# Kernel optimization log

Hardware: AMD Instinct MI355X
Metric: run time of the kernel (lower is better)

The kernel has to match this reference:

```python
import jax, jax.numpy as jnp
import numpy as np

N = 50000
E = 800000
D = 64


def _gcn_layer(x, row, col, norm, W, b, n_nodes):
    # h = X W  (PyG GCNConv applies linear before propagation, bias after)
    h = x @ W                                   # [N, D]
    msg = norm[:, None] * h[row]                # gather source feats, [E+N, D]
    out = jax.ops.segment_sum(msg, col, num_segments=n_nodes)  # scatter to targets
    return out + b


def _gcn_norm(edge_index, n_nodes, dtype):
    # add self loops with weight 1, symmetric normalization D^-1/2 (A+I) D^-1/2
    sl = jnp.arange(n_nodes, dtype=edge_index.dtype)
    row = jnp.concatenate([edge_index[0], sl])  # source
    col = jnp.concatenate([edge_index[1], sl])  # target
    w = jnp.ones(row.shape[0], dtype=dtype)
    deg = jax.ops.segment_sum(w, col, num_segments=n_nodes)
    dinv = jnp.where(deg > 0, jax.lax.rsqrt(deg), 0.0)
    norm = dinv[row] * dinv[col]                # [E+N]
    return row, col, norm


def setup_inputs() -> dict:
    key = jax.random.key(0)
    k1, k2, k3, k4 = jax.random.split(key, 4)
    x = jax.random.normal(k1, (N, D), dtype=jnp.float32)
    edge_index = jax.random.randint(k2, (2, E), 0, N, dtype=jnp.int64)
    # Glorot-style init like PyG GCNConv lin weights; bias zeros
    s = 1.0 / np.sqrt(D)
    W1 = jax.random.uniform(k3, (D, D), jnp.float32, -s, s)
    W2 = jax.random.uniform(k4, (D, D), jnp.float32, -s, s)
    b1 = jnp.zeros((D,), jnp.float32)
    b2 = jnp.zeros((D,), jnp.float32)
    return {"x": x, "W1": W1, "b1": b1, "W2": W2, "b2": b2, "edge_index": edge_index}


def reference(x, W1, b1, W2, b2, edge_index):
    n_nodes = x.shape[0]
    row, col, norm = _gcn_norm(edge_index, n_nodes, x.dtype)
    z = _gcn_layer(x, row, col, norm, W1, b1, n_nodes)
    z = jax.nn.relu(z)
    z = _gcn_layer(z, row, col, norm, W2, b2, n_nodes)
    z = jax.nn.relu(z)
    return z
```

## Files before the change

### kernel.cpp

```cpp
#include <hip/hip_runtime.h>


#define DF 64
#define XS_LD 68
#define ECHUNK 4096
#define BCAP 5120

__device__ __forceinline__ unsigned short f2bf(float f) {
  union { float f; unsigned int u; } c; c.f = f;
  unsigned int r = c.u + 0x7FFFu + ((c.u >> 16) & 1u);
  return (unsigned short)(r >> 16);
}
__device__ __forceinline__ float bflo(unsigned int u) {
  union { unsigned int u; float f; } c; c.u = u << 16; return c.f;
}
__device__ __forceinline__ float bfhi(unsigned int u) {
  union { unsigned int u; float f; } c; c.u = u & 0xFFFF0000u; return c.f;
}

__global__ void init_cur_k(int* __restrict__ gcursor) {
  gcursor[threadIdx.x] = threadIdx.x * BCAP;
}

__global__ __launch_bounds__(256) void part_k(
    const int* __restrict__ rows, const int* __restrict__ cols,
    int* __restrict__ gcursor, unsigned int* __restrict__ bfile, int e_cnt)
{
  __shared__ int h[256];
  __shared__ int p[256];
  __shared__ int lb[256];
  __shared__ int cur[256];
  __shared__ int gb[256];
  __shared__ unsigned int buf[ECHUNK];
  const int tid = threadIdx.x;
  h[tid] = 0; __syncthreads();

  const int e0 = blockIdx.x * ECHUNK;
  const int m  = min(ECHUNK, e_cnt - e0);
  unsigned int pk[ECHUNK / 256];
  int bk[ECHUNK / 256];
#pragma unroll
  for (int j = 0; j < ECHUNK / 256; ++j) {
    int idx = j * 256 + tid;
    if (idx < m) {
      int c = cols[e0 + idx];
      int r = rows[e0 + idx];
      bk[j] = c >> 8;
      pk[j] = ((unsigned int)(c & 255) << 16) | (unsigned int)r;
      atomicAdd(&h[bk[j]], 1);
    } else bk[j] = -1;
  }
  __syncthreads();

  const int myc = h[tid];
  p[tid] = myc; __syncthreads();
  for (int off = 1; off < 256; off <<= 1) {
    int t = (tid >= off) ? p[tid - off] : 0;
    __syncthreads();
    p[tid] += t;
    __syncthreads();
  }
  const int ex = p[tid] - myc;
  lb[tid] = ex; cur[tid] = ex;
  if (myc > 0) gb[tid] = atomicAdd(&gcursor[tid], myc);
  __syncthreads();

#pragma unroll
  for (int j = 0; j < ECHUNK / 256; ++j)
    if (bk[j] >= 0) { int pos = atomicAdd(&cur[bk[j]], 1); buf[pos] = pk[j]; }
  __syncthreads();

  for (int i = tid; i < m; i += 256) {
    int lo = 0, hi = 255;
    while (lo < hi) { int mid = (lo + hi + 1) >> 1; if (lb[mid] <= i) lo = mid; else hi = mid - 1; }
    bfile[gb[lo] + (i - lb[lo])] = buf[i];
  }
}

__global__ __launch_bounds__(256) void bucket_k(
    const unsigned int* __restrict__ bfile, const int* __restrict__ gcursor,
    int* __restrict__ csr_src, int* __restrict__ basep, int* __restrict__ cntp,
    float* __restrict__ dinv, int n)
{
  __shared__ unsigned int ein[BCAP];
  __shared__ unsigned short eout[BCAP];
  __shared__ int h[256];
  __shared__ int p[256];
  __shared__ int cur[256];
  const int tid = threadIdx.x;
  const int b   = blockIdx.x;
  const int s   = b * BCAP;
  int L = gcursor[b] - s;
  if (L > BCAP) L = BCAP;

  for (int i = tid; i < L; i += 256) ein[i] = bfile[s + i];
  h[tid] = 0; __syncthreads();
  for (int i = tid; i < L; i += 256) atomicAdd(&h[(ein[i] >> 16) & 255], 1);
  __syncthreads();

  const int myc = h[tid];
  p[tid] = myc; __syncthreads();
  for (int off = 1; off < 256; off <<= 1) {
    int t = (tid >= off) ? p[tid - off] : 0;
    __syncthreads();
    p[tid] += t;
    __syncthreads();
  }
  const int ex = p[tid] - myc;
  cur[tid] = ex;
  __syncthreads();

  for (int i = tid; i < L; i += 256) {
    unsigned int pk = ein[i];
    int pos = atomicAdd(&cur[(pk >> 16) & 255], 1);
    eout[pos] = (unsigned short)(pk & 0xffffu);
  }
  __syncthreads();

  for (int i = tid; i < L; i += 256) csr_src[s + i] = (int)eout[i];

  const int node = b * 256 + tid;
  if (node < n) {
    basep[node] = s + ex;
    cntp[node]  = myc;
    dinv[node]  = rsqrtf(1.0f + (float)myc);
  }
}

__global__ __launch_bounds__(256) void conv_k(
    const float* __restrict__ x, const float* __restrict__ dinv,
    uint4* __restrict__ xh, int n)
{
  int t = blockIdx.x * blockDim.x + threadIdx.x;
  if (t >= n * 8) return;
  const float dv = dinv[t >> 3];
  float4 v0 = ((const float4*)x)[(size_t)t * 2 + 0];
  float4 v1 = ((const float4*)x)[(size_t)t * 2 + 1];
  uint4 o;
  o.x = (unsigned int)f2bf(dv * v0.x) | ((unsigned int)f2bf(dv * v0.y) << 16);
  o.y = (unsigned int)f2bf(dv * v0.z) | ((unsigned int)f2bf(dv * v0.w) << 16);
  o.z = (unsigned int)f2bf(dv * v1.x) | ((unsigned int)f2bf(dv * v1.y) << 16);
  o.w = (unsigned int)f2bf(dv * v1.z) | ((unsigned int)f2bf(dv * v1.w) << 16);
  xh[t] = o;
}

template<int OUTBF>
__global__ __launch_bounds__(256) void fused_layer_k(
    const uint4* __restrict__ inh, const float* __restrict__ W,
    const float* __restrict__ bias, const int* __restrict__ csr_src,
    const int* __restrict__ basep, const int* __restrict__ cntp,
    const float* __restrict__ dinv, void* __restrict__ outp, int n)
{
  __shared__ float Ws[DF * XS_LD];
  __shared__ float Ss[32 * XS_LD];
  const int tid = threadIdx.x;

#pragma unroll
  for (int i = 0; i < 4; ++i) {
    const int f4 = tid + 256 * i;
    const int k  = f4 >> 4;
    const int c0 = (f4 & 15) * 4;
    *(float4*)(Ws + k * XS_LD + c0) = *(const float4*)(W + (size_t)f4 * 4);
  }

  const int nl   = tid >> 3;
  const int q    = tid & 7;
  const int node = blockIdx.x * 32 + nl;
  const bool valid = (node < n);
  float dv = 0.f;

  if (valid) {
    float a[8] = {0,0,0,0,0,0,0,0};
    float b2[8] = {0,0,0,0,0,0,0,0};
    dv = dinv[node];
    {
      uint4 v = inh[(size_t)node * 8 + q];
      a[0] += bflo(v.x); a[1] += bfhi(v.x); a[2] += bflo(v.y); a[3] += bfhi(v.y);
      a[4] += bflo(v.z); a[5] += bfhi(v.z); a[6] += bflo(v.w); a[7] += bfhi(v.w);
    }
    const int s = basep[node], c = cntp[node];
    int k = 0;
    for (; k + 4 <= c; k += 4) {
      int r0 = csr_src[s + k + 0], r1 = csr_src[s + k + 1];
      int r2 = csr_src[s + k + 2], r3 = csr_src[s + k + 3];
      uint4 v0 = inh[(size_t)r0 * 8 + q];
      uint4 v1 = inh[(size_t)r1 * 8 + q];
      uint4 v2 = inh[(size_t)r2 * 8 + q];
      uint4 v3 = inh[(size_t)r3 * 8 + q];
      a[0]  += bflo(v0.x) + bflo(v1.x); a[1]  += bfhi(v0.x) + bfhi(v1.x);
      a[2]  += bflo(v0.y) + bflo(v1.y); a[3]  += bfhi(v0.y) + bfhi(v1.y);
      a[4]  += bflo(v0.z) + bflo(v1.z); a[5]  += bfhi(v0.z) + bfhi(v1.z);
      a[6]  += bflo(v0.w) + bflo(v1.w); a[7]  += bfhi(v0.w) + bfhi(v1.w);
      b2[0] += bflo(v2.x) + bflo(v3.x); b2[1] += bfhi(v2.x) + bfhi(v3.x);
      b2[2] += bflo(v2.y) + bflo(v3.y); b2[3] += bfhi(v2.y) + bfhi(v3.y);
      b2[4] += bflo(v2.z) + bflo(v3.z); b2[5] += bfhi(v2.z) + bfhi(v3.z);
      b2[6] += bflo(v2.w) + bflo(v3.w); b2[7] += bfhi(v2.w) + bfhi(v3.w);
    }
    for (; k < c; ++k) {
      int r = csr_src[s + k];
      uint4 v = inh[(size_t)r * 8 + q];
      a[0] += bflo(v.x); a[1] += bfhi(v.x); a[2] += bflo(v.y); a[3] += bfhi(v.y);
      a[4] += bflo(v.z); a[5] += bfhi(v.z); a[6] += bflo(v.w); a[7] += bfhi(v.w);
    }
    float4 s0 = make_float4(dv * (a[0] + b2[0]), dv * (a[1] + b2[1]),
                            dv * (a[2] + b2[2]), dv * (a[3] + b2[3]));
    float4 s1 = make_float4(dv * (a[4] + b2[4]), dv * (a[5] + b2[5]),
                            dv * (a[6] + b2[6]), dv * (a[7] + b2[7]));
    *(float4*)(Ss + nl * XS_LD + q * 8 + 0) = s0;
    *(float4*)(Ss + nl * XS_LD + q * 8 + 4) = s1;
  }
  __syncthreads();

  float4 o0 = ((const float4*)bias)[q * 2 + 0];
  float4 o1 = ((const float4*)bias)[q * 2 + 1];
#pragma unroll 16
  for (int k = 0; k < DF; ++k) {
    const float sk = Ss[nl * XS_LD + k];
    const float4 w0 = *(const float4*)(Ws + k * XS_LD + q * 8 + 0);
    const float4 w1 = *(const float4*)(Ws + k * XS_LD + q * 8 + 4);
    o0.x += sk * w0.x; o0.y += sk * w0.y; o0.z += sk * w0.z; o0.w += sk * w0.w;
    o1.x += sk * w1.x; o1.y += sk * w1.y; o1.z += sk * w1.z; o1.w += sk * w1.w;
  }
  if (valid) {
    o0.x = fmaxf(o0.x, 0.f); o0.y = fmaxf(o0.y, 0.f);
    o0.z = fmaxf(o0.z, 0.f); o0.w = fmaxf(o0.w, 0.f);
    o1.x = fmaxf(o1.x, 0.f); o1.y = fmaxf(o1.y, 0.f);
    o1.z = fmaxf(o1.z, 0.f); o1.w = fmaxf(o1.w, 0.f);
    if (OUTBF) {
      uint4 u;
      u.x = (unsigned int)f2bf(dv * o0.x) | ((unsigned int)f2bf(dv * o0.y) << 16);
      u.y = (unsigned int)f2bf(dv * o0.z) | ((unsigned int)f2bf(dv * o0.w) << 16);
      u.z = (unsigned int)f2bf(dv * o1.x) | ((unsigned int)f2bf(dv * o1.y) << 16);
      u.w = (unsigned int)f2bf(dv * o1.z) | ((unsigned int)f2bf(dv * o1.w) << 16);
      ((uint4*)outp)[(size_t)node * 8 + q] = u;
    } else {
      ((float4*)outp)[(size_t)node * 16 + q * 2 + 0] = o0;
      ((float4*)outp)[(size_t)node * 16 + q * 2 + 1] = o1;
    }
  }
}

extern "C" void kernel_launch(void* const* d_in, const int* in_sizes, int n_in,
                              void* d_out, int out_size, void* d_ws, size_t ws_size,
                              hipStream_t stream) {
  const float* x  = (const float*)d_in[0];
  const float* W1 = (const float*)d_in[1];
  const float* b1 = (const float*)d_in[2];
  const float* W2 = (const float*)d_in[3];
  const float* b2 = (const float*)d_in[4];
  const int*   ei = (const int*)d_in[5];

  const int n = in_sizes[0] / DF;
  const int E = in_sizes[5] / 2;
  const int* rows = ei;
  const int* cols = ei + E;
  const int nb = (n + 255) >> 8;
  const int eblocks = (E + ECHUNK - 1) / ECHUNK;

  char* w = (char*)d_ws;
  size_t off = 0;
  auto alloc = [&](size_t bytes) { char* p = w + off; off = (off + bytes + 255) & ~(size_t)255; return p; };
  float* dinv    = (float*)alloc((size_t)n * 4);
  int*   cntp    = (int*)  alloc((size_t)n * 4);
  int*   basep   = (int*)  alloc((size_t)n * 4);
  int*   gcursor = (int*)  alloc(256 * 4);
  unsigned int* bfile = (unsigned int*)alloc((size_t)nb * BCAP * 4);
  int*   csr_src = (int*)  alloc((size_t)nb * BCAP * 4);
  uint4* xh      = (uint4*)alloc((size_t)n * DF * 2);
  uint4* zh      = (uint4*)alloc((size_t)n * DF * 2);

  const int b256 = 256;

  init_cur_k<<<1, 256, 0, stream>>>(gcursor);
  part_k<<<eblocks, b256, 0, stream>>>(rows, cols, gcursor, bfile, E);
  bucket_k<<<nb, b256, 0, stream>>>(bfile, gcursor, csr_src, basep, cntp, dinv, n);

  conv_k<<<(n * 8 + 255) / 256, b256, 0, stream>>>(x, dinv, xh, n);

  const int lay_blocks = (n + 31) / 32;

  fused_layer_k<1><<<lay_blocks, b256, 0, stream>>>(xh, W1, b1, csr_src, basep, cntp, dinv, zh, n);
  fused_layer_k<0><<<lay_blocks, b256, 0, stream>>>(zh, W2, b2, csr_src, basep, cntp, dinv, d_out, n);
}
```

Baseline: 93.53 us.

## Split bf16 features into column halves and gather each half in separate passes

```diff
diff --git a/kernel.cpp b/kernel.cpp
--- a/kernel.cpp
+++ b/kernel.cpp
@@ -5,6 +5,8 @@
 #define XS_LD 68
 #define ECHUNK 4096
 #define BCAP 5120
+
+typedef float vf4 __attribute__((ext_vector_type(4)));
 
 __device__ __forceinline__ unsigned short f2bf(float f) {
   union { float f; unsigned int u; } c; c.f = f;
@@ -46,7 +48,7 @@
       int c = cols[e0 + idx];
       int r = rows[e0 + idx];
       bk[j] = c >> 8;
-      pk[j] = ((unsigned int)(c & 255) << 16) | (unsigned int)r;
+      pk[j] = ((unsigned int)bk[j] << 24) | ((unsigned int)(c & 255) << 16) | (unsigned int)r;
       atomicAdd(&h[bk[j]], 1);
     } else bk[j] = -1;
   }
@@ -71,9 +73,9 @@
   __syncthreads();
 
   for (int i = tid; i < m; i += 256) {
-    int lo = 0, hi = 255;
-    while (lo < hi) { int mid = (lo + hi + 1) >> 1; if (lb[mid] <= i) lo = mid; else hi = mid - 1; }
-    bfile[gb[lo] + (i - lb[lo])] = buf[i];
+    unsigned int v = buf[i];
+    int b = (int)(v >> 24);
+    bfile[gb[b] + (i - lb[b])] = v;
   }
 }
 
@@ -129,11 +131,12 @@
 
 __global__ __launch_bounds__(256) void conv_k(
     const float* __restrict__ x, const float* __restrict__ dinv,
-    uint4* __restrict__ xh, int n)
+    uint4* __restrict__ xlo, uint4* __restrict__ xhi, int n)
 {
   int t = blockIdx.x * blockDim.x + threadIdx.x;
   if (t >= n * 8) return;
-  const float dv = dinv[t >> 3];
+  const int node = t >> 3, q = t & 7;
+  const float dv = dinv[node];
   float4 v0 = ((const float4*)x)[(size_t)t * 2 + 0];
   float4 v1 = ((const float4*)x)[(size_t)t * 2 + 1];
   uint4 o;
@@ -141,101 +144,165 @@
   o.y = (unsigned int)f2bf(dv * v0.z) | ((unsigned int)f2bf(dv * v0.w) << 16);
   o.z = (unsigned int)f2bf(dv * v1.x) | ((unsigned int)f2bf(dv * v1.y) << 16);
   o.w = (unsigned int)f2bf(dv * v1.z) | ((unsigned int)f2bf(dv * v1.w) << 16);
-  xh[t] = o;
+  if (q < 4) xlo[(size_t)node * 4 + q] = o;
+  else       xhi[(size_t)node * 4 + (q - 4)] = o;
+}
+
+__global__ __launch_bounds__(256) void gatherA_k(
+    const uint4* __restrict__ inlo, const int* __restrict__ csr_src,
+    const int* __restrict__ basep, const int* __restrict__ cntp,
+    const float* __restrict__ dinv, float* __restrict__ Slo, int n)
+{
+  const int nl = threadIdx.x >> 2;
+  const int q  = threadIdx.x & 3;
+  const int node = blockIdx.x * 64 + nl;
+  if (node >= n) return;
+
+  float a[8], b[8];
+  {
+    uint4 v = inlo[(size_t)node * 4 + q];
+    a[0] = bflo(v.x); a[1] = bfhi(v.x); a[2] = bflo(v.y); a[3] = bfhi(v.y);
+    a[4] = bflo(v.z); a[5] = bfhi(v.z); a[6] = bflo(v.w); a[7] = bfhi(v.w);
+#pragma unroll
+    for (int j = 0; j < 8; ++j) b[j] = 0.f;
+  }
+  const int s = basep[node], c = cntp[node];
+  int k = 0;
+  for (; k + 4 <= c; k += 4) {
+    int r0 = __builtin_nontemporal_load(csr_src + s + k + 0);
+    int r1 = __builtin_nontemporal_load(csr_src + s + k + 1);
+    int r2 = __builtin_nontemporal_load(csr_src + s + k + 2);
+    int r3 = __builtin_nontemporal_load(csr_src + s + k + 3);
+    uint4 v0 = inlo[(size_t)r0 * 4 + q];
+    uint4 v1 = inlo[(size_t)r1 * 4 + q];
+    uint4 v2 = inlo[(size_t)r2 * 4 + q];
+    uint4 v3 = inlo[(size_t)r3 * 4 + q];
+    a[0] += bflo(v0.x) + bflo(v1.x); a[1] += bfhi(v0.x) + bfhi(v1.x);
+    a[2] += bflo(v0.y) + bflo(v1.y); a[3] += bfhi(v0.y) + bfhi(v1.y);
+    a[4] += bflo(v0.z) + bflo(v1.z); a[5] += bfhi(v0.z) + bfhi(v1.z);
+    a[6] += bflo(v0.w) + bflo(v1.w); a[7] += bfhi(v0.w) + bfhi(v1.w);
+    b[0] += bflo(v2.x) + bflo(v3.x); b[1] += bfhi(v2.x) + bfhi(v3.x);
+    b[2] += bflo(v2.y) + bflo(v3.y); b[3] += bfhi(v2.y) + bfhi(v3.y);
+    b[4] += bflo(v2.z) + bflo(v3.z); b[5] += bfhi(v2.z) + bfhi(v3.z);
+    b[6] += bflo(v2.w) + bflo(v3.w); b[7] += bfhi(v2.w) + bfhi(v3.w);
+  }
+  for (; k < c; ++k) {
+    int r = __builtin_nontemporal_load(csr_src + s + k);
+    uint4 v = inlo[(size_t)r * 4 + q];
+    a[0] += bflo(v.x); a[1] += bfhi(v.x); a[2] += bflo(v.y); a[3] += bfhi(v.y);
+    a[4] += bflo(v.z); a[5] += bfhi(v.z); a[6] += bflo(v.w); a[7] += bfhi(v.w);
+  }
+  const float dv = dinv[node];
+  vf4 o0 = {dv*(a[0]+b[0]), dv*(a[1]+b[1]), dv*(a[2]+b[2]), dv*(a[3]+b[3])};
+  vf4 o1 = {dv*(a[4]+b[4]), dv*(a[5]+b[5]), dv*(a[6]+b[6]), dv*(a[7]+b[7])};
+  __builtin_nontemporal_store(o0, (vf4*)(Slo + (size_t)node * 32 + q * 8 + 0));
+  __builtin_nontemporal_store(o1, (vf4*)(Slo + (size_t)node * 32 + q * 8 + 4));
 }
 
 template<int OUTBF>
-__global__ __launch_bounds__(256) void fused_layer_k(
-    const uint4* __restrict__ inh, const float* __restrict__ W,
-    const float* __restrict__ bias, const int* __restrict__ csr_src,
-    const int* __restrict__ basep, const int* __restrict__ cntp,
-    const float* __restrict__ dinv, void* __restrict__ outp, int n)
+__global__ __launch_bounds__(256) void gatherB_gemm_k(
+    const uint4* __restrict__ inhi, const float* __restrict__ Slo,
+    const float* __restrict__ W, const float* __restrict__ bias,
+    const int* __restrict__ csr_src, const int* __restrict__ basep,
+    const int* __restrict__ cntp, const float* __restrict__ dinv,
+    void* __restrict__ out0, void* __restrict__ out1, int n)
 {
   __shared__ float Ws[DF * XS_LD];
-  __shared__ float Ss[32 * XS_LD];
+  __shared__ float Ss[64 * XS_LD];
   const int tid = threadIdx.x;
 
 #pragma unroll
   for (int i = 0; i < 4; ++i) {
     const int f4 = tid + 256 * i;
-    const int k  = f4 >> 4;
+    const int kk = f4 >> 4;
     const int c0 = (f4 & 15) * 4;
-    *(float4*)(Ws + k * XS_LD + c0) = *(const float4*)(W + (size_t)f4 * 4);
-  }
-
-  const int nl   = tid >> 3;
-  const int q    = tid & 7;
-  const int node = blockIdx.x * 32 + nl;
-  const bool valid = (node < n);
-  float dv = 0.f;
-
-  if (valid) {
-    float a[8] = {0,0,0,0,0,0,0,0};
-    float b2[8] = {0,0,0,0,0,0,0,0};
-    dv = dinv[node];
+    *(float4*)(Ws + kk * XS_LD + c0) = *(const float4*)(W + (size_t)f4 * 4);
+  }
+
+  const int nl = tid >> 2;
+  const int q  = tid & 3;
+  const int node = blockIdx.x * 64 + nl;
+
+  if (node < n) {
+    float a[8], b[8];
     {
-      uint4 v = inh[(size_t)node * 8 + q];
-      a[0] += bflo(v.x); a[1] += bfhi(v.x); a[2] += bflo(v.y); a[3] += bfhi(v.y);
-      a[4] += bflo(v.z); a[5] += bfhi(v.z); a[6] += bflo(v.w); a[7] += bfhi(v.w);
+      uint4 v = inhi[(size_t)node * 4 + q];
+      a[0] = bflo(v.x); a[1] = bfhi(v.x); a[2] = bflo(v.y); a[3] = bfhi(v.y);
+      a[4] = bflo(v.z); a[5] = bfhi(v.z); a[6] = bflo(v.w); a[7] = bfhi(v.w);
+#pragma unroll
+      for (int j = 0; j < 8; ++j) b[j] = 0.f;
     }
     const int s = basep[node], c = cntp[node];
     int k = 0;
     for (; k + 4 <= c; k += 4) {
-      int r0 = csr_src[s + k + 0], r1 = csr_src[s + k + 1];
-      int r2 = csr_src[s + k + 2], r3 = csr_src[s + k + 3];
-      uint4 v0 = inh[(size_t)r0 * 8 + q];
-      uint4 v1 = inh[(size_t)r1 * 8 + q];
-      uint4 v2 = inh[(size_t)r2 * 8 + q];
-      uint4 v3 = inh[(size_t)r3 * 8 + q];
-      a[0]  += bflo(v0.x) + bflo(v1.x); a[1]  += bfhi(v0.x) + bfhi(v1.x);
-      a[2]  += bflo(v0.y) + bflo(v1.y); a[3]  += bfhi(v0.y) + bfhi(v1.y);
-      a[4]  += bflo(v0.z) + bflo(v1.z); a[5]  += bfhi(v0.z) + bfhi(v1.z);
-      a[6]  += bflo(v0.w) + bflo(v1.w); a[7]  += bfhi(v0.w) + bfhi(v1.w);
-      b2[0] += bflo(v2.x) + bflo(v3.x); b2[1] += bfhi(v2.x) + bfhi(v3.x);
-      b2[2] += bflo(v2.y) + bflo(v3.y); b2[3] += bfhi(v2.y) + bfhi(v3.y);
-      b2[4] += bflo(v2.z) + bflo(v3.z); b2[5] += bfhi(v2.z) + bfhi(v3.z);
-      b2[6] += bflo(v2.w) + bflo(v3.w); b2[7] += bfhi(v2.w) + bfhi(v3.w);
+      int r0 = __builtin_nontemporal_load(csr_src + s + k + 0);
+      int r1 = __builtin_nontemporal_load(csr_src + s + k + 1);
+      int r2 = __builtin_nontemporal_load(csr_src + s + k + 2);
+      int r3 = __builtin_nontemporal_load(csr_src + s + k + 3);
+      uint4 v0 = inhi[(size_t)r0 * 4 + q];
+      uint4 v1 = inhi[(size_t)r1 * 4 + q];
+      uint4 v2 = inhi[(size_t)r2 * 4 + q];
+      uint4 v3 = inhi[(size_t)r3 * 4 + q];
+      a[0] += bflo(v0.x) + bflo(v1.x); a[1] += bfhi(v0.x) + bfhi(v1.x);
+      a[2] += bflo(v0.y) + bflo(v1.y); a[3] += bfhi(v0.y) + bfhi(v1.y);
+      a[4] += bflo(v0.z) + bflo(v1.z); a[5] += bfhi(v0.z) + bfhi(v1.z);
+      a[6] += bflo(v0.w) + bflo(v1.w); a[7] += bfhi(v0.w) + bfhi(v1.w);
+      b[0] += bflo(v2.x) + bflo(v3.x); b[1] += bfhi(v2.x) + bfhi(v3.x);
+      b[2] += bflo(v2.y) + bflo(v3.y); b[3] += bfhi(v2.y) + bfhi(v3.y);
+      b[4] += bflo(v2.z) + bflo(v3.z); b[5] += bfhi(v2.z) + bfhi(v3.z);
+      b[6] += bflo(v2.w) + bflo(v3.w); b[7] += bfhi(v2.w) + bfhi(v3.w);
     }
     for (; k < c; ++k) {
-      int r = csr_src[s + k];
-      uint4 v = inh[(size_t)r * 8 + q];
+      int r = __builtin_nontemporal_load(csr_src + s + k);
+      uint4 v = inhi[(size_t)r * 4 + q];
       a[0] += bflo(v.x); a[1] += bfhi(v.x); a[2] += bflo(v.y); a[3] += bfhi(v.y);
       a[4] += bflo(v.z); a[5] += bfhi(v.z); a[6] += bflo(v.w); a[7] += bfhi(v.w);
     }
-    float4 s0 = make_float4(dv * (a[0] + b2[0]), dv * (a[1] + b2[1]),
-                            dv * (a[2] + b2[2]), dv * (a[3] + b2[3]));
-    float4 s1 = make_float4(dv * (a[4] + b2[4]), dv * (a[5] + b2[5]),
-                            dv * (a[6] + b2[6]), dv * (a[7] + b2[7]));
-    *(float4*)(Ss + nl * XS_LD + q * 8 + 0) = s0;
-    *(float4*)(Ss + nl * XS_LD + q * 8 + 4) = s1;
-  }
-  __syncthreads();
-
-  float4 o0 = ((const float4*)bias)[q * 2 + 0];
-  float4 o1 = ((const float4*)bias)[q * 2 + 1];
+    const float dv = dinv[node];
+    float4 h0 = make_float4(dv*(a[0]+b[0]), dv*(a[1]+b[1]), dv*(a[2]+b[2]), dv*(a[3]+b[3]));
+    float4 h1 = make_float4(dv*(a[4]+b[4]), dv*(a[5]+b[5]), dv*(a[6]+b[6]), dv*(a[7]+b[7]));
+    *(float4*)(Ss + nl * XS_LD + 32 + q * 8 + 0) = h0;
+    *(float4*)(Ss + nl * XS_LD + 32 + q * 8 + 4) = h1;
+    vf4 l0 = __builtin_nontemporal_load((const vf4*)(Slo + (size_t)node * 32 + q * 8 + 0));
+    vf4 l1 = __builtin_nontemporal_load((const vf4*)(Slo + (size_t)node * 32 + q * 8 + 4));
+    *(vf4*)(Ss + nl * XS_LD + q * 8 + 0) = l0;
+    *(vf4*)(Ss + nl * XS_LD + q * 8 + 4) = l1;
+  }
+  __syncthreads();
+
+  const int q2 = tid & 7;
+#pragma unroll
+  for (int sub = 0; sub < 2; ++sub) {
+    const int nl2 = (tid >> 3) + 32 * sub;
+    const int node2 = blockIdx.x * 64 + nl2;
+    float4 o0 = ((const float4*)bias)[q2 * 2 + 0];
+    float4 o1 = ((const float4*)bias)[q2 * 2 + 1];
 #pragma unroll 16
-  for (int k = 0; k < DF; ++k) {
-    const float sk = Ss[nl * XS_LD + k];
-    const float4 w0 = *(const float4*)(Ws + k * XS_LD + q * 8 + 0);
-    const float4 w1 = *(const float4*)(Ws + k * XS_LD + q * 8 + 4);
-    o0.x += sk * w0.x; o0.y += sk * w0.y; o0.z += sk * w0.z; o0.w += sk * w0.w;
-    o1.x += sk * w1.x; o1.y += sk * w1.y; o1.z += sk * w1.z; o1.w += sk * w1.w;
-  }
-  if (valid) {
-    o0.x = fmaxf(o0.x, 0.f); o0.y = fmaxf(o0.y, 0.f);
-    o0.z = fmaxf(o0.z, 0.f); o0.w = fmaxf(o0.w, 0.f);
-    o1.x = fmaxf(o1.x, 0.f); o1.y = fmaxf(o1.y, 0.f);
-    o1.z = fmaxf(o1.z, 0.f); o1.w = fmaxf(o1.w, 0.f);
-    if (OUTBF) {
-      uint4 u;
-      u.x = (unsigned int)f2bf(dv * o0.x) | ((unsigned int)f2bf(dv * o0.y) << 16);
-      u.y = (unsigned int)f2bf(dv * o0.z) | ((unsigned int)f2bf(dv * o0.w) << 16);
-      u.z = (unsigned int)f2bf(dv * o1.x) | ((unsigned int)f2bf(dv * o1.y) << 16);
-      u.w = (unsigned int)f2bf(dv * o1.z) | ((unsigned int)f2bf(dv * o1.w) << 16);
-      ((uint4*)outp)[(size_t)node * 8 + q] = u;
-    } else {
-      ((float4*)outp)[(size_t)node * 16 + q * 2 + 0] = o0;
-      ((float4*)outp)[(size_t)node * 16 + q * 2 + 1] = o1;
+    for (int k = 0; k < DF; ++k) {
+      const float sk = Ss[nl2 * XS_LD + k];
+      const float4 w0 = *(const float4*)(Ws + k * XS_LD + q2 * 8 + 0);
+      const float4 w1 = *(const float4*)(Ws + k * XS_LD + q2 * 8 + 4);
+      o0.x += sk * w0.x; o0.y += sk * w0.y; o0.z += sk * w0.z; o0.w += sk * w0.w;
+      o1.x += sk * w1.x; o1.y += sk * w1.y; o1.z += sk * w1.z; o1.w += sk * w1.w;
+    }
+    if (node2 < n) {
+      o0.x = fmaxf(o0.x, 0.f); o0.y = fmaxf(o0.y, 0.f);
+      o0.z = fmaxf(o0.z, 0.f); o0.w = fmaxf(o0.w, 0.f);
+      o1.x = fmaxf(o1.x, 0.f); o1.y = fmaxf(o1.y, 0.f);
+      o1.z = fmaxf(o1.z, 0.f); o1.w = fmaxf(o1.w, 0.f);
+      if (OUTBF) {
+        const float dv2 = dinv[node2];
+        uint4 u;
+        u.x = (unsigned int)f2bf(dv2 * o0.x) | ((unsigned int)f2bf(dv2 * o0.y) << 16);
+        u.y = (unsigned int)f2bf(dv2 * o0.z) | ((unsigned int)f2bf(dv2 * o0.w) << 16);
+        u.z = (unsigned int)f2bf(dv2 * o1.x) | ((unsigned int)f2bf(dv2 * o1.y) << 16);
+        u.w = (unsigned int)f2bf(dv2 * o1.z) | ((unsigned int)f2bf(dv2 * o1.w) << 16);
+        if (q2 < 4) ((uint4*)out0)[(size_t)node2 * 4 + q2] = u;
+        else        ((uint4*)out1)[(size_t)node2 * 4 + (q2 - 4)] = u;
+      } else {
+        ((float4*)out0)[(size_t)node2 * 16 + q2 * 2 + 0] = o0;
+        ((float4*)out0)[(size_t)node2 * 16 + q2 * 2 + 1] = o1;
+      }
     }
   }
 }
@@ -266,8 +333,11 @@
   int*   gcursor = (int*)  alloc(256 * 4);
   unsigned int* bfile = (unsigned int*)alloc((size_t)nb * BCAP * 4);
   int*   csr_src = (int*)  alloc((size_t)nb * BCAP * 4);
-  uint4* xh      = (uint4*)alloc((size_t)n * DF * 2);
-  uint4* zh      = (uint4*)alloc((size_t)n * DF * 2);
+  uint4* xh_lo   = (uint4*)alloc((size_t)n * 64);
+  uint4* xh_hi   = (uint4*)alloc((size_t)n * 64);
+  uint4* zh_lo   = (uint4*)alloc((size_t)n * 64);
+  uint4* zh_hi   = (uint4*)alloc((size_t)n * 64);
+  float* Slo     = (float*)alloc((size_t)n * 32 * 4);
 
   const int b256 = 256;
 
@@ -275,10 +345,12 @@
   part_k<<<eblocks, b256, 0, stream>>>(rows, cols, gcursor, bfile, E);
   bucket_k<<<nb, b256, 0, stream>>>(bfile, gcursor, csr_src, basep, cntp, dinv, n);
 
-  conv_k<<<(n * 8 + 255) / 256, b256, 0, stream>>>(x, dinv, xh, n);
-
-  const int lay_blocks = (n + 31) / 32;
-
-  fused_layer_k<1><<<lay_blocks, b256, 0, stream>>>(xh, W1, b1, csr_src, basep, cntp, dinv, zh, n);
-  fused_layer_k<0><<<lay_blocks, b256, 0, stream>>>(zh, W2, b2, csr_src, basep, cntp, dinv, d_out, n);
-}
+  conv_k<<<(n * 8 + 255) / 256, b256, 0, stream>>>(x, dinv, xh_lo, xh_hi, n);
+
+  const int gblocks = (n + 63) / 64;
+
+  gatherA_k<<<gblocks, b256, 0, stream>>>(xh_lo, csr_src, basep, cntp, dinv, Slo, n);
+  gatherB_gemm_k<1><<<gblocks, b256, 0, stream>>>(xh_hi, Slo, W1, b1, csr_src, basep, cntp, dinv, zh_lo, zh_hi, n);
+  gatherA_k<<<gblocks, b256, 0, stream>>>(zh_lo, csr_src, basep, cntp, dinv, Slo, n);
+  gatherB_gemm_k<0><<<gblocks, b256, 0, stream>>>(zh_hi, Slo, W2, b2, csr_src, basep, cntp, dinv, d_out, nullptr, n);
+}
```

New measurement: 146.6 us. 56.8% more time.

## Sort nodes by degree within buckets and drop binary search in partition scatter

Applied to the files above, without the earlier changes.

```diff
diff --git a/kernel.cpp b/kernel.cpp
--- a/kernel.cpp
+++ b/kernel.cpp
@@ -46,7 +46,7 @@
       int c = cols[e0 + idx];
       int r = rows[e0 + idx];
       bk[j] = c >> 8;
-      pk[j] = ((unsigned int)(c & 255) << 16) | (unsigned int)r;
+      pk[j] = ((unsigned int)bk[j] << 24) | ((unsigned int)(c & 255) << 16) | (unsigned int)r;
       atomicAdd(&h[bk[j]], 1);
     } else bk[j] = -1;
   }
@@ -71,22 +71,24 @@
   __syncthreads();
 
   for (int i = tid; i < m; i += 256) {
-    int lo = 0, hi = 255;
-    while (lo < hi) { int mid = (lo + hi + 1) >> 1; if (lb[mid] <= i) lo = mid; else hi = mid - 1; }
-    bfile[gb[lo] + (i - lb[lo])] = buf[i];
+    unsigned int v = buf[i];
+    int b = (int)(v >> 24);
+    bfile[gb[b] + (i - lb[b])] = v;
   }
 }
 
 __global__ __launch_bounds__(256) void bucket_k(
     const unsigned int* __restrict__ bfile, const int* __restrict__ gcursor,
     int* __restrict__ csr_src, int* __restrict__ basep, int* __restrict__ cntp,
-    float* __restrict__ dinv, int n)
+    float* __restrict__ dinv, int* __restrict__ perm, int n)
 {
   __shared__ unsigned int ein[BCAP];
   __shared__ unsigned short eout[BCAP];
   __shared__ int h[256];
   __shared__ int p[256];
   __shared__ int cur[256];
+  __shared__ int h2[64];
+  __shared__ int c2[64];
   const int tid = threadIdx.x;
   const int b   = blockIdx.x;
   const int s   = b * BCAP;
@@ -94,7 +96,9 @@
   if (L > BCAP) L = BCAP;
 
   for (int i = tid; i < L; i += 256) ein[i] = bfile[s + i];
-  h[tid] = 0; __syncthreads();
+  h[tid] = 0;
+  if (tid < 64) h2[tid] = 0;
+  __syncthreads();
   for (int i = tid; i < L; i += 256) atomicAdd(&h[(ein[i] >> 16) & 255], 1);
   __syncthreads();
 
@@ -120,10 +124,24 @@
   for (int i = tid; i < L; i += 256) csr_src[s + i] = (int)eout[i];
 
   const int node = b * 256 + tid;
-  if (node < n) {
+  const bool valid = (node < n);
+  int cap = 0;
+  if (valid) {
     basep[node] = s + ex;
     cntp[node]  = myc;
     dinv[node]  = rsqrtf(1.0f + (float)myc);
+    cap = min(myc, 63);
+    atomicAdd(&h2[cap], 1);
+  }
+  __syncthreads();
+  if (tid == 0) {
+    int run = 0;
+    for (int i = 0; i < 64; ++i) { c2[i] = run; run += h2[i]; }
+  }
+  __syncthreads();
+  if (valid) {
+    int r = atomicAdd(&c2[cap], 1);
+    perm[b * 256 + r] = node;
   }
 }
 
@@ -149,10 +167,12 @@
     const uint4* __restrict__ inh, const float* __restrict__ W,
     const float* __restrict__ bias, const int* __restrict__ csr_src,
     const int* __restrict__ basep, const int* __restrict__ cntp,
-    const float* __restrict__ dinv, void* __restrict__ outp, int n)
+    const float* __restrict__ dinv, const int* __restrict__ perm,
+    void* __restrict__ outp, int n)
 {
   __shared__ float Ws[DF * XS_LD];
   __shared__ float Ss[32 * XS_LD];
+  __shared__ int   nd[32];
   const int tid = threadIdx.x;
 
 #pragma unroll
@@ -165,8 +185,10 @@
 
   const int nl   = tid >> 3;
   const int q    = tid & 7;
-  const int node = blockIdx.x * 32 + nl;
-  const bool valid = (node < n);
+  const int idx  = blockIdx.x * 32 + nl;
+  const bool valid = (idx < n);
+  const int node = valid ? perm[idx] : 0;
+  if (q == 0) nd[nl] = node;
   float dv = 0.f;
 
   if (valid) {
@@ -181,8 +203,10 @@
     const int s = basep[node], c = cntp[node];
     int k = 0;
     for (; k + 4 <= c; k += 4) {
-      int r0 = csr_src[s + k + 0], r1 = csr_src[s + k + 1];
-      int r2 = csr_src[s + k + 2], r3 = csr_src[s + k + 3];
+      int r0 = __builtin_nontemporal_load(csr_src + s + k + 0);
+      int r1 = __builtin_nontemporal_load(csr_src + s + k + 1);
+      int r2 = __builtin_nontemporal_load(csr_src + s + k + 2);
+      int r3 = __builtin_nontemporal_load(csr_src + s + k + 3);
       uint4 v0 = inh[(size_t)r0 * 8 + q];
       uint4 v1 = inh[(size_t)r1 * 8 + q];
       uint4 v2 = inh[(size_t)r2 * 8 + q];
@@ -197,7 +221,7 @@
       b2[6] += bflo(v2.w) + bflo(v3.w); b2[7] += bfhi(v2.w) + bfhi(v3.w);
     }
     for (; k < c; ++k) {
-      int r = csr_src[s + k];
+      int r = __builtin_nontemporal_load(csr_src + s + k);
       uint4 v = inh[(size_t)r * 8 + q];
       a[0] += bflo(v.x); a[1] += bfhi(v.x); a[2] += bflo(v.y); a[3] += bfhi(v.y);
       a[4] += bflo(v.z); a[5] += bfhi(v.z); a[6] += bflo(v.w); a[7] += bfhi(v.w);
@@ -263,6 +287,7 @@
   float* dinv    = (float*)alloc((size_t)n * 4);
   int*   cntp    = (int*)  alloc((size_t)n * 4);
   int*   basep   = (int*)  alloc((size_t)n * 4);
+  int*   permp   = (int*)  alloc((size_t)n * 4);
   int*   gcursor = (int*)  alloc(256 * 4);
   unsigned int* bfile = (unsigned int*)alloc((size_t)nb * BCAP * 4);
   int*   csr_src = (int*)  alloc((size_t)nb * BCAP * 4);
@@ -273,12 +298,12 @@
 
   init_cur_k<<<1, 256, 0, stream>>>(gcursor);
   part_k<<<eblocks, b256, 0, stream>>>(rows, cols, gcursor, bfile, E);
-  bucket_k<<<nb, b256, 0, stream>>>(bfile, gcursor, csr_src, basep, cntp, dinv, n);
+  bucket_k<<<nb, b256, 0, stream>>>(bfile, gcursor, csr_src, basep, cntp, dinv, permp, n);
 
   conv_k<<<(n * 8 + 255) / 256, b256, 0, stream>>>(x, dinv, xh, n);
 
   const int lay_blocks = (n + 31) / 32;
 
-  fused_layer_k<1><<<lay_blocks, b256, 0, stream>>>(xh, W1, b1, csr_src, basep, cntp, dinv, zh, n);
-  fused_layer_k<0><<<lay_blocks, b256, 0, stream>>>(zh, W2, b2, csr_src, basep, cntp, dinv, d_out, n);
-}
+  fused_layer_k<1><<<lay_blocks, b256, 0, stream>>>(xh, W1, b1, csr_src, basep, cntp, dinv, permp, zh, n);
+  fused_layer_k<0><<<lay_blocks, b256, 0, stream>>>(zh, W2, b2, csr_src, basep, cntp, dinv, permp, d_out, n);
+}
```

After: 102.2 us. 9.2% more time.
